# Kernel tuning notes

Measured on AMD Instinct MI355X. Metric: run time of the kernel, lower is better.

Reference implementation:

```python
import jax, jax.numpy as jnp
import numpy as np

NUM_FIELDS = 16
EMBED = 256
BATCH = 2048
NUM_PAIRS = NUM_FIELDS * (NUM_FIELDS - 1) // 2  # 120


def setup_inputs() -> dict:
    key = jax.random.key(0)
    k1, k2, k3 = jax.random.split(key, 3)
    emb_inputs = jax.random.normal(k1, (BATCH, NUM_FIELDS, EMBED), dtype=jnp.float32)
    bound = 1.0 / np.sqrt(NUM_PAIRS)  # torch: 1/sqrt(weight.size(0)) = 1/sqrt(in_features)
    weight = jax.random.uniform(k2, (NUM_PAIRS, EMBED, EMBED), dtype=jnp.float32,
                                minval=-bound, maxval=bound)
    bias = jax.random.uniform(k3, (NUM_PAIRS, EMBED), dtype=jnp.float32,
                              minval=-bound, maxval=bound)
    return {"emb_inputs": emb_inputs, "weight": weight, "bias": bias}


def reference(emb_inputs, weight, bias):
    # Pair indices (i, j) with i < j over fields
    row_idx, col_idx = np.triu_indices(NUM_FIELDS, k=1)  # each length NUM_PAIRS
    p = emb_inputs[:, row_idx]  # (B, P, E)
    q = emb_inputs[:, col_idx]  # (B, P, E)
    # FieldEachTypeBilinear: (p @ W_p) * q + b_p, per-pair weight W_p (E, E)
    out = jnp.einsum('bpe,pef->bpf', p, weight) * q + bias  # (B, P, E)
    return out
```

## Files before the change

### kernel.cpp

```cpp
#include <hip/hip_runtime.h>
#include <hip/hip_bf16.h>
#include <stdint.h>

#define BATCH   2048
#define NF      16
#define EMBED   256
#define NPAIRS  120
#define OUTROW  (NPAIRS*EMBED)
#define EMBROW  (NF*EMBED)

typedef __attribute__((ext_vector_type(8))) __bf16 bf16x8;
typedef __attribute__((ext_vector_type(4))) float  f32x4;

typedef __attribute__((address_space(3))) void       lds_void;
typedef const __attribute__((address_space(1))) void g_void;

__device__ __forceinline__ unsigned short f2bf(float f) {
    unsigned u = __float_as_uint(f);
    u += 0x7FFF + ((u >> 16) & 1);
    return (unsigned short)(u >> 16);
}

__device__ __forceinline__ void pair_rc(int p, int& r, int& c) {
    int rr = 0, base = 0;
    while (p >= base + (NF - 1 - rr)) { base += NF - 1 - rr; ++rr; }
    r = rr; c = rr + 1 + (p - base);
}

__global__ __launch_bounds__(256) void emb_permute(const float* __restrict__ emb,
                                                   unsigned short* __restrict__ embp) {
    __shared__ float tile[64][65];
    const int b0 = blockIdx.x * 64;
    const int e0 = blockIdx.y * 64;
    const int f  = blockIdx.z;
    const int t  = threadIdx.x;
#pragma unroll
    for (int rnd = 0; rnd < 4; ++rnd) {
        int bl = rnd * 16 + (t >> 4);
        int el = (t & 15) * 4;
        const float4 v = *(const float4*)(emb + (size_t)(b0 + bl) * EMBROW + f * EMBED + e0 + el);
        tile[bl][el] = v.x; tile[bl][el + 1] = v.y; tile[bl][el + 2] = v.z; tile[bl][el + 3] = v.w;
    }
    __syncthreads();
#pragma unroll
    for (int rnd = 0; rnd < 2; ++rnd) {
        int ec = rnd * 4 + (t >> 6);
        int bl = t & 63;
        unsigned short h[8];
#pragma unroll
        for (int i = 0; i < 8; ++i) h[i] = f2bf(tile[bl][ec * 8 + i]);
        uint4 w;
        w.x = h[0] | ((unsigned)h[1] << 16);
        w.y = h[2] | ((unsigned)h[3] << 16);
        w.z = h[4] | ((unsigned)h[5] << 16);
        w.w = h[6] | ((unsigned)h[7] << 16);
        *(uint4*)(embp + (size_t)f * (32u * BATCH * 8) + (size_t)(e0 / 8 + ec) * (BATCH * 8)
                        + (size_t)(b0 + bl) * 8) = w;
    }
}

__global__ __launch_bounds__(256) void wt_permute(const float* __restrict__ wt,
                                                  unsigned short* __restrict__ wtp) {
    __shared__ float tile[64][65];
    const int e0 = blockIdx.x * 64;
    const int f0 = blockIdx.y * 64;
    const int p  = blockIdx.z;
    const int t  = threadIdx.x;
#pragma unroll
    for (int rnd = 0; rnd < 4; ++rnd) {
        int el = rnd * 16 + (t >> 4);
        int fl = (t & 15) * 4;
        const float4 v = *(const float4*)(wt + (size_t)p * (EMBED * EMBED) + (size_t)(e0 + el) * EMBED + f0 + fl);
        tile[el][fl] = v.x; tile[el][fl + 1] = v.y; tile[el][fl + 2] = v.z; tile[el][fl + 3] = v.w;
    }
    __syncthreads();
#pragma unroll
    for (int rnd = 0; rnd < 2; ++rnd) {
        int ec = rnd * 4 + (t >> 6);
        int fl = t & 63;
        unsigned short h[8];
#pragma unroll
        for (int i = 0; i < 8; ++i) h[i] = f2bf(tile[ec * 8 + i][fl]);
        uint4 w;
        w.x = h[0] | ((unsigned)h[1] << 16);
        w.y = h[2] | ((unsigned)h[3] << 16);
        w.z = h[4] | ((unsigned)h[5] << 16);
        w.w = h[6] | ((unsigned)h[7] << 16);
        *(uint4*)(wtp + (size_t)p * (EMBED * EMBED) + (size_t)(e0 / 8 + ec) * (EMBED * 8)
                       + (size_t)(f0 + fl) * 8) = w;
    }
}

__global__ __launch_bounds__(256) void bilinear_main(
        const float* __restrict__ emb, const float* __restrict__ bias,
        const unsigned short* __restrict__ embp, const unsigned short* __restrict__ wtp,
        float* __restrict__ out) {
    __shared__ __align__(16) unsigned short a_lds[4 * 128 * 8];
    __shared__ __align__(16) unsigned short b_lds[4 * 128 * 8];
    __shared__ __align__(16) float ep[4][16 * 66];

    const int nblk = blockIdx.x, mblk = blockIdx.y, p = blockIdx.z;
    int r, c; pair_rc(p, r, c);
    const int m0 = mblk * 128, n0 = nblk * 128;
    const int t = threadIdx.x;
    const int wave = t >> 6, lane = t & 63;
    const int wm = (wave >> 1) * 64, wn = (wave & 1) * 64;
    const int kq = lane >> 4, l15 = lane & 15;

    const unsigned short* a_base = embp + (size_t)r * (32u * BATCH * 8);
    const unsigned short* b_base = wtp + (size_t)p * (EMBED * EMBED);

    f32x4 acc[4][4] = {};

#pragma unroll 1
    for (int ki = 0; ki < 8; ++ki) {
#pragma unroll
        for (int i = 0; i < 2; ++i) {
            int q  = i * 256 + t;
            int kc = q >> 7, xl = q & 127;
            const unsigned short* ga = a_base + (size_t)(ki * 4 + kc) * (BATCH * 8) + (size_t)(m0 + xl) * 8;
            __builtin_amdgcn_global_load_lds((g_void*)ga, (lds_void*)(a_lds + q * 8), 16, 0, 0);
            const unsigned short* gb = b_base + (size_t)(ki * 4 + kc) * (EMBED * 8) + (size_t)(n0 + xl) * 8;
            __builtin_amdgcn_global_load_lds((g_void*)gb, (lds_void*)(b_lds + q * 8), 16, 0, 0);
        }
        __syncthreads();

        bf16x8 af[4], bfr[4];
#pragma unroll
        for (int i = 0; i < 4; ++i)
            af[i] = *(const bf16x8*)(a_lds + (kq * 128 + wm + i * 16 + l15) * 8);
#pragma unroll
        for (int j = 0; j < 4; ++j)
            bfr[j] = *(const bf16x8*)(b_lds + (kq * 128 + wn + j * 16 + l15) * 8);
#pragma unroll
        for (int i = 0; i < 4; ++i)
#pragma unroll
            for (int j = 0; j < 4; ++j)
                acc[i][j] = __builtin_amdgcn_mfma_f32_16x16x32_bf16(af[i], bfr[j], acc[i][j], 0, 0, 0);
        __syncthreads();
    }

    const int lrow4 = lane >> 4;
    const int lcol  = (lane & 15) * 4;
    const f32x4 bv = *(const f32x4*)(bias + p * EMBED + n0 + wn + lcol);

#pragma unroll
    for (int i = 0; i < 4; ++i) {
#pragma unroll
        for (int j = 0; j < 4; ++j)
#pragma unroll
            for (int reg = 0; reg < 4; ++reg)
                ep[wave][(kq * 4 + reg) * 66 + j * 16 + l15] = acc[i][j][reg];
#pragma unroll
        for (int rr = 0; rr < 4; ++rr) {
            const int lrow = rr * 4 + lrow4;
            const f32x4 v = *(const f32x4*)&ep[wave][lrow * 66 + lcol];
            const int row  = m0 + wm + i * 16 + lrow;
            const f32x4 q = *(const f32x4*)(emb + (size_t)row * EMBROW + c * EMBED + n0 + wn + lcol);
            f32x4 o = v * q + bv;
            __builtin_nontemporal_store(o, (f32x4*)(out + (size_t)row * OUTROW + p * EMBED + n0 + wn + lcol));
        }
    }
}

extern "C" void kernel_launch(void* const* d_in, const int* in_sizes, int n_in,
                              void* d_out, int out_size, void* d_ws, size_t ws_size,
                              hipStream_t stream) {
    const float* emb    = (const float*)d_in[0];
    const float* weight = (const float*)d_in[1];
    const float* bias   = (const float*)d_in[2];
    float* out = (float*)d_out;

    unsigned short* wtp  = (unsigned short*)d_ws;
    unsigned short* embp = (unsigned short*)((char*)d_ws + 15728640);

    wt_permute<<<dim3(4, 4, NPAIRS), 256, 0, stream>>>(weight, wtp);
    emb_permute<<<dim3(BATCH / 64, EMBED / 64, NF), 256, 0, stream>>>(emb, embp);
    bilinear_main<<<dim3(2, BATCH / 128, NPAIRS), 256, 0, stream>>>(emb, bias, embp, wtp, out);
}
```

Baseline: 342.2 us.

## Triple-buffer LDS K-loop with async global-to-LDS prefetch and manual waitcnt

Replaces the single-buffered K loop in the bilinear GEMM with a fully unrolled three-stage LDS ring. Global-to-LDS loads for future K slices are issued while the MFMAs run on the current slice, with explicit vmcnt waits and barriers. The epilogue staging buffer now reuses the A LDS region, which keeps LDS use in check, and launch bounds request 3 blocks per CU. The aim is to hide global load latency behind compute, at the cost of more LDS, hand-tuned waitcnt values that must match the issue count, and tighter register limits.

```diff
diff --git a/kernel.cpp b/kernel.cpp
--- a/kernel.cpp
+++ b/kernel.cpp
@@ -91,13 +91,12 @@
     }
 }
 
-__global__ __launch_bounds__(256) void bilinear_main(
+__global__ __launch_bounds__(256, 3) void bilinear_main(
         const float* __restrict__ emb, const float* __restrict__ bias,
         const unsigned short* __restrict__ embp, const unsigned short* __restrict__ wtp,
         float* __restrict__ out) {
-    __shared__ __align__(16) unsigned short a_lds[4 * 128 * 8];
-    __shared__ __align__(16) unsigned short b_lds[4 * 128 * 8];
-    __shared__ __align__(16) float ep[4][16 * 66];
+    __shared__ __align__(16) unsigned short a_lds[3][4096];
+    __shared__ __align__(16) unsigned short b_lds[3][4096];
 
     const int nblk = blockIdx.x, mblk = blockIdx.y, p = blockIdx.z;
     int r, c; pair_rc(p, r, c);
@@ -112,34 +111,73 @@
 
     f32x4 acc[4][4] = {};
 
-#pragma unroll 1
-    for (int ki = 0; ki < 8; ++ki) {
-#pragma unroll
-        for (int i = 0; i < 2; ++i) {
-            int q  = i * 256 + t;
-            int kc = q >> 7, xl = q & 127;
-            const unsigned short* ga = a_base + (size_t)(ki * 4 + kc) * (BATCH * 8) + (size_t)(m0 + xl) * 8;
-            __builtin_amdgcn_global_load_lds((g_void*)ga, (lds_void*)(a_lds + q * 8), 16, 0, 0);
-            const unsigned short* gb = b_base + (size_t)(ki * 4 + kc) * (EMBED * 8) + (size_t)(n0 + xl) * 8;
-            __builtin_amdgcn_global_load_lds((g_void*)gb, (lds_void*)(b_lds + q * 8), 16, 0, 0);
-        }
-        __syncthreads();
-
-        bf16x8 af[4], bfr[4];
-#pragma unroll
-        for (int i = 0; i < 4; ++i)
-            af[i] = *(const bf16x8*)(a_lds + (kq * 128 + wm + i * 16 + l15) * 8);
-#pragma unroll
-        for (int j = 0; j < 4; ++j)
-            bfr[j] = *(const bf16x8*)(b_lds + (kq * 128 + wn + j * 16 + l15) * 8);
-#pragma unroll
-        for (int i = 0; i < 4; ++i)
-#pragma unroll
-            for (int j = 0; j < 4; ++j)
-                acc[i][j] = __builtin_amdgcn_mfma_f32_16x16x32_bf16(af[i], bfr[j], acc[i][j], 0, 0, 0);
-        __syncthreads();
-    }
-
+#define STAGE(buf, ki)                                                              \
+    {                                                                               \
+        _Pragma("unroll")                                                           \
+        for (int i = 0; i < 2; ++i) {                                               \
+            int q  = i * 256 + t;                    \
+            int kc = q >> 7, xl = q & 127;                                          \
+            const unsigned short* ga = a_base + (size_t)((ki) * 4 + kc) * (BATCH * 8) \
+                                             + (size_t)(m0 + xl) * 8;               \
+            __builtin_amdgcn_global_load_lds((g_void*)ga,                           \
+                (lds_void*)(&a_lds[buf][0] + q * 8), 16, 0, 0);                     \
+            const unsigned short* gb = b_base + (size_t)((ki) * 4 + kc) * (EMBED * 8) \
+                                             + (size_t)(n0 + xl) * 8;               \
+            __builtin_amdgcn_global_load_lds((g_void*)gb,                           \
+                (lds_void*)(&b_lds[buf][0] + q * 8), 16, 0, 0);                     \
+        }                                                                           \
+    }
+
+#define COMPUTE(buf)                                                                \
+    {                                                                               \
+        bf16x8 af[4], bfr[4];                                                       \
+        _Pragma("unroll")                                                           \
+        for (int i = 0; i < 4; ++i)                                                 \
+            af[i] = *(const bf16x8*)(&a_lds[buf][0] + (kq * 128 + wm + i * 16 + l15) * 8); \
+        _Pragma("unroll")                                                           \
+        for (int j = 0; j < 4; ++j)                                                 \
+            bfr[j] = *(const bf16x8*)(&b_lds[buf][0] + (kq * 128 + wn + j * 16 + l15) * 8); \
+        _Pragma("unroll")                                                           \
+        for (int i = 0; i < 4; ++i)                                                 \
+            _Pragma("unroll")                                                       \
+            for (int j = 0; j < 4; ++j)                                             \
+                acc[i][j] = __builtin_amdgcn_mfma_f32_16x16x32_bf16(af[i], bfr[j], acc[i][j], 0, 0, 0); \
+    }
+
+#define FENCE asm volatile("" ::: "memory")
+#define SBAR  __builtin_amdgcn_sched_barrier(0)
+#define BAR()                                                                       \
+    {                                                                               \
+        SBAR;                                                                       \
+        asm volatile("s_waitcnt lgkmcnt(0)" ::: "memory");                          \
+        SBAR;                                                                       \
+        __builtin_amdgcn_s_barrier();                                               \
+        SBAR;                                                                       \
+    }
+#define WAITVM(N)                                                                   \
+    {                                                                               \
+        SBAR;                                                                       \
+        asm volatile("s_waitcnt vmcnt(" #N ")" ::: "memory");                       \
+        SBAR;                                                                       \
+    }
+
+    STAGE(0, 0) FENCE; SBAR;
+    STAGE(1, 1) FENCE; SBAR;
+    STAGE(2, 2) FENCE; SBAR;
+    WAITVM(0) BAR();
+
+                           COMPUTE(0) BAR();
+    STAGE(0, 3) WAITVM(8) BAR(); COMPUTE(1) BAR();
+    STAGE(1, 4) WAITVM(8) BAR(); COMPUTE(2) BAR();
+    STAGE(2, 5) WAITVM(8) BAR(); COMPUTE(0) BAR();
+    STAGE(0, 6) WAITVM(8) BAR(); COMPUTE(1) BAR();
+    STAGE(1, 7) WAITVM(8) BAR(); COMPUTE(2) BAR();
+                WAITVM(4) BAR(); COMPUTE(0) BAR();
+                WAITVM(0) BAR(); COMPUTE(1)
+
+    __syncthreads();
+
+    float* epw = (float*)(&a_lds[0][0]) + wave * (16 * 66);
     const int lrow4 = lane >> 4;
     const int lcol  = (lane & 15) * 4;
     const f32x4 bv = *(const f32x4*)(bias + p * EMBED + n0 + wn + lcol);
@@ -150,17 +188,23 @@
         for (int j = 0; j < 4; ++j)
 #pragma unroll
             for (int reg = 0; reg < 4; ++reg)
-                ep[wave][(kq * 4 + reg) * 66 + j * 16 + l15] = acc[i][j][reg];
+                epw[(kq * 4 + reg) * 66 + j * 16 + l15] = acc[i][j][reg];
 #pragma unroll
         for (int rr = 0; rr < 4; ++rr) {
             const int lrow = rr * 4 + lrow4;
-            const f32x4 v = *(const f32x4*)&ep[wave][lrow * 66 + lcol];
+            const f32x4 v = *(const f32x4*)&epw[lrow * 66 + lcol];
             const int row  = m0 + wm + i * 16 + lrow;
             const f32x4 q = *(const f32x4*)(emb + (size_t)row * EMBROW + c * EMBED + n0 + wn + lcol);
             f32x4 o = v * q + bv;
             __builtin_nontemporal_store(o, (f32x4*)(out + (size_t)row * OUTROW + p * EMBED + n0 + wn + lcol));
         }
     }
+#undef STAGE
+#undef COMPUTE
+#undef FENCE
+#undef SBAR
+#undef BAR
+#undef WAITVM
 }
 
 extern "C" void kernel_launch(void* const* d_in, const int* in_sizes, int n_in,
```

Result: no change. 338.5 us (-1.1%).
